# Kernel optimization log

Measured on AMD Instinct MI355X. Metric: run time of the kernel, lower is better.

## Reference

```python
import jax, jax.numpy as jnp
import numpy as np

N_NODES = 400      # total nodes across batch
B = 10             # graphs in batch (40 nodes each)
N_CONFIGS = 1000   # fixed by tile dataset
CONFIG_FEAT_DIM = 24
NODE_FEAT_DIM = 85  # continuous cols; node_feat has +1 col for shape-ele-type idx
N_SHAPE_TYPES = 8
SHAPE_EMB = 4
N_OPS = 120
OP_EMB = 32
H = 64             # h_dim
E = 800            # edges
CAT_DIM = NODE_FEAT_DIM + SHAPE_EMB + OP_EMB + CONFIG_FEAT_DIM  # 145


def _lin(k, i, o):
    return jax.random.normal(k, (i, o), jnp.float32) * (1.0 / np.sqrt(i))


def setup_inputs() -> dict:
    key = jax.random.key(0)
    ks = jax.random.split(key, 32)
    node_cont = jax.random.normal(ks[0], (N_NODES, NODE_FEAT_DIM), jnp.float32)
    shape_type = jax.random.randint(ks[1], (N_NODES, 1), 0, N_SHAPE_TYPES).astype(jnp.float32)
    node_feat = jnp.concatenate([node_cont, shape_type], axis=-1)  # [N, 86]
    node_opcode = jax.random.randint(ks[2], (N_NODES,), 0, N_OPS)
    config_feat = jax.random.normal(ks[3], (B * N_CONFIGS, CONFIG_FEAT_DIM), jnp.float32)
    edge_index = jax.random.randint(ks[4], (2, E), 0, N_NODES)
    batch = jnp.arange(N_NODES) // (N_NODES // B)  # 40 nodes per graph
    inp = dict(
        node_feat=node_feat, node_opcode=node_opcode, config_feat=config_feat,
        edge_index=edge_index, batch=batch,
        op_emb=jax.random.normal(ks[5], (N_OPS, OP_EMB), jnp.float32),
        shape_emb=jax.random.normal(ks[6], (N_SHAPE_TYPES, SHAPE_EMB), jnp.float32),
        W1=_lin(ks[7], CAT_DIM, 2 * H), b1=jnp.zeros((2 * H,), jnp.float32),
        W2=_lin(ks[8], 2 * H, 2 * H), b2=jnp.zeros((2 * H,), jnp.float32),
        Wl0=_lin(ks[9], 2 * H, H), Wr0=_lin(ks[10], 2 * H, H), bg0=jnp.zeros((H,), jnp.float32),
        Wl1=_lin(ks[11], H, H), Wr1=_lin(ks[12], H, H), bg1=jnp.zeros((H,), jnp.float32),
        Wl2=_lin(ks[13], H, H), Wr2=_lin(ks[14], H, H), bg2=jnp.zeros((H,), jnp.float32),
        Wp1=_lin(ks[15], H, H // 2), bp1=jnp.zeros((H // 2,), jnp.float32),
        Wp2=_lin(ks[16], H // 2, 1), bp2=jnp.zeros((1,), jnp.float32),
    )
    return inp


def _sage(x, src, dst, Wl, Wr, b, n):
    # PyG SAGEConv: lin_l(x) + lin_r(mean_{j->i} x_j), applied over [N, C, D]
    agg = jax.ops.segment_sum(x[src], dst, num_segments=n)
    deg = jax.ops.segment_sum(jnp.ones((src.shape[0],), x.dtype), dst, num_segments=n)
    mean = agg / jnp.maximum(deg, 1.0)[:, None, None]
    return x @ Wl + mean @ Wr + b


def reference(node_feat, node_opcode, config_feat, edge_index, batch,
              op_emb, shape_emb, W1, b1, W2, b2,
              Wl0, Wr0, bg0, Wl1, Wr1, bg1, Wl2, Wr2, bg2,
              Wp1, bp1, Wp2, bp2):
    n = node_feat.shape[0]
    cfg = config_feat.reshape(-1, N_CONFIGS, CONFIG_FEAT_DIM)  # [B, 1000, 24]
    ste = shape_emb[node_feat[:, -1].astype(jnp.int32)]        # [N, 4]
    op = op_emb[node_opcode]                                   # [N, 32]
    xn = jnp.concatenate([node_feat[:, :-1], ste, op], axis=-1)  # [N, 121]
    xn = jnp.broadcast_to(xn[:, None, :], (n, N_CONFIGS, xn.shape[-1]))
    xc = cfg[batch]  # repeat_interleave(cfg, n_nodes, dim=0) -> per-node config
    x = jnp.concatenate([xn, xc], axis=-1)                     # [N, 1000, 145]
    x = jax.nn.relu(x @ W1 + b1)
    x = jax.nn.relu(x @ W2 + b2)                               # [N, 1000, 128]
    src, dst = edge_index[0], edge_index[1]
    for Wl, Wr, bg in ((Wl0, Wr0, bg0), (Wl1, Wr1, bg1), (Wl2, Wr2, bg2)):
        x = jax.nn.relu(_sage(x, src, dst, Wl, Wr, bg, n))     # [N, 1000, 64]
    xf = x.reshape(n, -1)                                      # [N, 64000]
    cnt = jax.ops.segment_sum(jnp.ones((n,), xf.dtype), batch, num_segments=B)
    xg = jax.ops.segment_max(xf, batch, num_segments=B) \
         + jax.ops.segment_sum(xf, batch, num_segments=B) / jnp.maximum(cnt, 1.0)[:, None]
    xg = xg.reshape(B, N_CONFIGS, -1)                          # [B, 1000, 64]
    xg = xg / jnp.linalg.norm(xg, axis=-1, keepdims=True)
    out = (jax.nn.relu(xg @ Wp1 + bp1) @ Wp2 + bp2)[..., 0]    # [B, 1000]
    return out
```

## Files before the change

### kernel.cpp

```cpp
#include <hip/hip_runtime.h>
#include <hip/hip_bf16.h>

typedef unsigned short u16;
typedef short bf16x8 __attribute__((ext_vector_type(8)));
typedef float f32x4 __attribute__((ext_vector_type(4)));

#define NN 400
#define NB 10
#define NC 1000
#define CFD 24
#define NFD 85
#define NFROW 86
#define SEDIM 4
#define OEDIM 32
#define XND 121
#define EE 800
#define N_SHAPE_GUARD 7

__device__ __forceinline__ float b2f(u16 u) { return __uint_as_float((unsigned)u << 16); }
__device__ __forceinline__ u16 f2b(float v) {
  unsigned x = __float_as_uint(v);
  return (u16)((x + 0x7fff + ((x >> 16) & 1)) >> 16);
}
__device__ __forceinline__ float ldf(const void* p, int idx, int fz) {
  if (fz) return ((const float*)p)[idx];
  return b2f(((const u16*)p)[idx]);
}
__device__ __forceinline__ void stf(void* p, int idx, int fz, float v) {
  if (fz) { ((float*)p)[idx] = v; return; }
  ((u16*)p)[idx] = f2b(v);
}

__device__ __forceinline__ void detect_wave0(const void* W1, int t, int* flagl) {
  if (t < 64) {
    int wild = 0;
    const u16* wv = (const u16*)W1;
    for (int j = t; j < 512; j += 64) {
      float a = fabsf(b2f(wv[j]));
      if (!(a < 1e4f)) wild++;
    }
    #pragma unroll
    for (int off = 32; off; off >>= 1) wild += __shfl_xor(wild, off);
    if (t == 0) *flagl = (wild > 16) ? 1 : 0;
  }
}

__global__ __launch_bounds__(256) void k_prep_all(
    const void* __restrict__ node_feat, const int* __restrict__ opcode,
    const void* __restrict__ cfg, const int* __restrict__ edge_index,
    const void* __restrict__ op_emb, const void* __restrict__ shape_emb,
    const void* __restrict__ W1, const void* __restrict__ b1,
    const void* __restrict__ W2,
    const void* __restrict__ Wl0, const void* __restrict__ Wr0,
    const void* __restrict__ Wl1, const void* __restrict__ Wr1,
    const void* __restrict__ Wl2, const void* __restrict__ Wr2,
    float* __restrict__ A_node, float* __restrict__ C_cfg,
    u16* __restrict__ W2t, u16* __restrict__ Wc0t,
    u16* __restrict__ Wc1t, u16* __restrict__ Wc2t,
    int* __restrict__ offs, int* __restrict__ srcl) {
  __shared__ int flagl;
  int t = threadIdx.x;
  detect_wave0(W1, t, &flagl);
  __syncthreads();
  int fz = flagl;
  int bid = blockIdx.x;

  if (bid < 313) {
    __shared__ float w1l[CFD * 128];
    __shared__ float cfl[32 * CFD];
    int r0 = bid * 32;
    for (int idx = t; idx < CFD * 128; idx += 256)
      w1l[idx] = ldf(W1, (XND + (idx >> 7)) * 128 + (idx & 127), fz);
    for (int idx = t; idx < 32 * CFD; idx += 256) {
      int r = idx / CFD, k = idx - r * CFD;
      if (r0 + r < 10000) cfl[idx] = ldf(cfg, (r0 + r) * CFD + k, fz);
    }
    __syncthreads();
    for (int idx = t; idx < 4096; idx += 256) {
      int row = idx >> 7, col = idx & 127;
      if (r0 + row < 10000) {
        float acc = 0.f;
        #pragma unroll
        for (int k = 0; k < CFD; k++) acc += cfl[row * CFD + k] * w1l[k * 128 + col];
        C_cfg[(size_t)(r0 + row) * 128 + col] = acc;
      }
    }
    return;
  }
  if (bid < 363) {
    __shared__ float w1m[XND * 128];
    __shared__ float xnl[8 * 128];
    int i0 = (bid - 313) * 8;
    for (int idx = t; idx < XND * 128; idx += 256) w1m[idx] = ldf(W1, idx, fz);
    for (int idx = t; idx < 1024; idx += 256) {
      int node = idx >> 7, tt = idx & 127;
      int i = i0 + node;
      float v = 0.f;
      if (tt < NFD) {
        v = ldf(node_feat, i * NFROW + tt, fz);
      } else if (tt < NFD + SEDIM) {
        int st = (int)ldf(node_feat, i * NFROW + NFD, fz);
        st = min(max(st, 0), N_SHAPE_GUARD);
        v = ldf(shape_emb, st * SEDIM + (tt - NFD), fz);
      } else if (tt < XND) {
        int oc = min(max(opcode[i], 0), 119);
        v = ldf(op_emb, oc * OEDIM + (tt - NFD - SEDIM), fz);
      }
      xnl[idx] = v;
    }
    __syncthreads();
    for (int idx = t; idx < 1024; idx += 256) {
      int node = idx >> 7, tt = idx & 127;
      int i = i0 + node;
      float acc = ldf(b1, tt, fz);
      for (int k = 0; k < XND; k++) acc += xnl[node * 128 + k] * w1m[k * 128 + tt];
      A_node[i * 128 + tt] = acc;
    }
    return;
  }
  if (bid < 555) {
    int idx = (bid - 363) * 256 + t;
    if (idx < 16384) {
      int n = idx >> 7, k = idx & 127;
      W2t[idx] = f2b(ldf(W2, k * 128 + n, fz)); return;
    }
    idx -= 16384;
    if (idx < 16384) {
      int n = idx >> 7, k = idx & 127;
      float v = (n < 64) ? ldf(Wl0, k * 64 + n, fz) : ldf(Wr0, k * 64 + n - 64, fz);
      Wc0t[idx] = f2b(v); return;
    }
    idx -= 16384;
    if (idx < 8192) {
      int n = idx >> 6, k = idx & 63;
      float v = (n < 64) ? ldf(Wl1, k * 64 + n, fz) : ldf(Wr1, k * 64 + n - 64, fz);
      Wc1t[idx] = f2b(v); return;
    }
    idx -= 8192;
    if (idx < 8192) {
      int n = idx >> 6, k = idx & 63;
      float v = (n < 64) ? ldf(Wl2, k * 64 + n, fz) : ldf(Wr2, k * 64 + n - 64, fz);
      Wc2t[idx] = f2b(v); return;
    }
    return;
  }
  {
    __shared__ int cnt[NN];
    __shared__ int offl[NN + 1];
    for (int i = t; i < NN; i += 256) cnt[i] = 0;
    __syncthreads();
    for (int e = t; e < EE; e += 256) {
      int d = edge_index[EE + e] & 511; if (d < NN) atomicAdd(&cnt[d], 1);
    }
    __syncthreads();
    if (t == 0) {
      int s = 0;
      for (int i = 0; i < NN; i++) { offl[i] = s; s += cnt[i]; }
      offl[NN] = s;
    }
    __syncthreads();
    for (int i = t; i < NN; i += 256) cnt[i] = offl[i];
    for (int i = t; i < NN + 1; i += 256) offs[i] = offl[i];
    __syncthreads();
    for (int e = t; e < EE; e += 256) {
      int d = edge_index[EE + e] & 511;
      if (d < NN) {
        int p = atomicAdd(&cnt[d], 1);
        srcl[p] = min(max(edge_index[e], 0), NN - 1);
      }
    }
  }
}

__global__ __launch_bounds__(512, 1) void k_fused(
    const float* __restrict__ A_node, const float* __restrict__ C_cfg,
    const int* __restrict__ batch, const int* __restrict__ offs,
    const int* __restrict__ srcl,
    const u16* __restrict__ W2t, const u16* __restrict__ Wc0t,
    const u16* __restrict__ Wc1t, const u16* __restrict__ Wc2t,
    const void* __restrict__ b2, const void* __restrict__ bg0,
    const void* __restrict__ bg1, const void* __restrict__ bg2,
    const void* __restrict__ Wp1, const void* __restrict__ bp1,
    const void* __restrict__ Wp2, const void* __restrict__ bp2,
    const void* __restrict__ W1d, void* __restrict__ out) {
  __shared__ __align__(16) u16 xbuf[400 * 128];
  __shared__ __align__(16) u16 ybuf[400 * 64];
  __shared__ int offsl[401];
  __shared__ int srcll[EE];
  __shared__ int flagl;

  int c = blockIdx.x;
  int t = threadIdx.x;
  int w = t >> 6, l = t & 63;
  int lm = l & 15, quad = l >> 4;

  detect_wave0(W1d, t, &flagl);
  float* cfgl = (float*)ybuf;
  for (int idx = t; idx < 1280; idx += 512)
    cfgl[idx] = C_cfg[((size_t)(idx >> 7) * NC + c) * 128 + (idx & 127)];
  for (int idx = t; idx < 401; idx += 512) offsl[idx] = offs[idx];
  for (int idx = t; idx < EE; idx += 512) srcll[idx] = srcl[idx];
  __syncthreads();
  int fz = flagl;

  {
    bf16x8 wf[8][4];
    #pragma unroll
    for (int mt = 0; mt < 8; mt++)
      #pragma unroll
      for (int kt = 0; kt < 4; kt++)
        wf[mt][kt] = *reinterpret_cast<const bf16x8*>(W2t + (mt*16 + lm)*128 + kt*32 + quad*8);
    float bv[8][4];
    #pragma unroll
    for (int mt = 0; mt < 8; mt++)
      #pragma unroll
      for (int rg = 0; rg < 4; rg++) bv[mt][rg] = ldf(b2, mt*16 + quad*4 + rg, fz);

    for (int tile = w; tile < 25; tile += 8) {
      int i = tile*16 + lm;
      int b = batch[i] % NB;
      const float* an = A_node + i*128;
      const float* cf = cfgl + b*128;
      bf16x8 bfr[4];
      #pragma unroll
      for (int kt = 0; kt < 4; kt++) {
        int ko = kt*32 + quad*8;
        float4 a0 = *(const float4*)(an + ko);
        float4 a1 = *(const float4*)(an + ko + 4);
        float4 c0 = *(const float4*)(cf + ko);
        float4 c1 = *(const float4*)(cf + ko + 4);
        bf16x8 f;
        f[0] = (short)f2b(fmaxf(a0.x + c0.x, 0.f));
        f[1] = (short)f2b(fmaxf(a0.y + c0.y, 0.f));
        f[2] = (short)f2b(fmaxf(a0.z + c0.z, 0.f));
        f[3] = (short)f2b(fmaxf(a0.w + c0.w, 0.f));
        f[4] = (short)f2b(fmaxf(a1.x + c1.x, 0.f));
        f[5] = (short)f2b(fmaxf(a1.y + c1.y, 0.f));
        f[6] = (short)f2b(fmaxf(a1.z + c1.z, 0.f));
        f[7] = (short)f2b(fmaxf(a1.w + c1.w, 0.f));
        bfr[kt] = f;
      }
      f32x4 acc[8] = {};
      #pragma unroll
      for (int kt = 0; kt < 4; kt++)
        #pragma unroll
        for (int mt = 0; mt < 8; mt++)
          acc[mt] = __builtin_amdgcn_mfma_f32_16x16x32_bf16(wf[mt][kt], bfr[kt], acc[mt], 0, 0, 0);
      #pragma unroll
      for (int mt = 0; mt < 8; mt++) {
        ushort4 s;
        s.x = f2b(fmaxf(acc[mt][0] + bv[mt][0], 0.f));
        s.y = f2b(fmaxf(acc[mt][1] + bv[mt][1], 0.f));
        s.z = f2b(fmaxf(acc[mt][2] + bv[mt][2], 0.f));
        s.w = f2b(fmaxf(acc[mt][3] + bv[mt][3], 0.f));
        int ch = mt*2 + (quad >> 1);
        int chs = ch ^ (i & 7);
        *reinterpret_cast<ushort4*>(&xbuf[i*128 + chs*8 + (quad & 1)*4]) = s;
      }
    }
  }
  __syncthreads();

  {
    bf16x8 wl[4][4], wr[4][4];
    #pragma unroll
    for (int mt = 0; mt < 4; mt++)
      #pragma unroll
      for (int kt = 0; kt < 4; kt++) {
        wl[mt][kt] = *reinterpret_cast<const bf16x8*>(Wc0t + (mt*16 + lm)*128 + kt*32 + quad*8);
        wr[mt][kt] = *reinterpret_cast<const bf16x8*>(Wc0t + (64 + mt*16 + lm)*128 + kt*32 + quad*8);
      }
    float bv[4][4];
    #pragma unroll
    for (int mt = 0; mt < 4; mt++)
      #pragma unroll
      for (int rg = 0; rg < 4; rg++) bv[mt][rg] = ldf(bg0, mt*16 + quad*4 + rg, fz);

    for (int tile = w; tile < 25; tile += 8) {
      int i = tile*16 + lm;
      int o0 = offsl[i], o1 = offsl[i + 1];
      float rd = 1.f / fmaxf((float)(o1 - o0), 1.f);
      bf16x8 xf[4], mf[4];
      #pragma unroll
      for (int kt = 0; kt < 4; kt++)
        xf[kt] = *reinterpret_cast<const bf16x8*>(&xbuf[i*128 + ((kt*4 + quad) ^ (i & 7))*8]);
      float s8[4][8] = {};
      int e = o0;
      for (; e + 1 < o1; e += 2) {
        int sn0 = srcll[e], sn1 = srcll[e + 1];
        bf16x8 z0[4], z1[4];
        #pragma unroll
        for (int kt = 0; kt < 4; kt++) {
          z0[kt] = *reinterpret_cast<const bf16x8*>(&xbuf[sn0*128 + ((kt*4 + quad) ^ (sn0 & 7))*8]);
          z1[kt] = *reinterpret_cast<const bf16x8*>(&xbuf[sn1*128 + ((kt*4 + quad) ^ (sn1 & 7))*8]);
        }
        #pragma unroll
        for (int kt = 0; kt < 4; kt++)
          #pragma unroll
          for (int j = 0; j < 8; j++) {
            s8[kt][j] += b2f((u16)z0[kt][j]);
            s8[kt][j] += b2f((u16)z1[kt][j]);
          }
      }
      if (e < o1) {
        int sn0 = srcll[e];
        #pragma unroll
        for (int kt = 0; kt < 4; kt++) {
          bf16x8 zv = *reinterpret_cast<const bf16x8*>(&xbuf[sn0*128 + ((kt*4 + quad) ^ (sn0 & 7))*8]);
          #pragma unroll
          for (int j = 0; j < 8; j++) s8[kt][j] += b2f((u16)zv[j]);
        }
      }
      #pragma unroll
      for (int kt = 0; kt < 4; kt++) {
        bf16x8 f;
        #pragma unroll
        for (int j = 0; j < 8; j++) f[j] = (short)f2b(s8[kt][j] * rd);
        mf[kt] = f;
      }
      f32x4 acc[4] = {};
      #pragma unroll
      for (int kt = 0; kt < 4; kt++)
        #pragma unroll
        for (int mt = 0; mt < 4; mt++) {
          acc[mt] = __builtin_amdgcn_mfma_f32_16x16x32_bf16(wl[mt][kt], xf[kt], acc[mt], 0, 0, 0);
          acc[mt] = __builtin_amdgcn_mfma_f32_16x16x32_bf16(wr[mt][kt], mf[kt], acc[mt], 0, 0, 0);
        }
      #pragma unroll
      for (int mt = 0; mt < 4; mt++) {
        ushort4 s;
        s.x = f2b(fmaxf(acc[mt][0] + bv[mt][0], 0.f));
        s.y = f2b(fmaxf(acc[mt][1] + bv[mt][1], 0.f));
        s.z = f2b(fmaxf(acc[mt][2] + bv[mt][2], 0.f));
        s.w = f2b(fmaxf(acc[mt][3] + bv[mt][3], 0.f));
        int ch = mt*2 + (quad >> 1);
        int chs = ch ^ (i & 7);
        *reinterpret_cast<ushort4*>(&ybuf[i*64 + chs*8 + (quad & 1)*4]) = s;
      }
    }
  }
  __syncthreads();

  u16* src_buf = ybuf;
  u16* dst_buf = xbuf;
  for (int layer = 0; layer < 2; layer++) {
    const u16* Wt = (layer == 0) ? Wc1t : Wc2t;
    const void* bg = (layer == 0) ? bg1 : bg2;
    bf16x8 wl[4][2], wr[4][2];
    #pragma unroll
    for (int mt = 0; mt < 4; mt++)
      #pragma unroll
      for (int kt = 0; kt < 2; kt++) {
        wl[mt][kt] = *reinterpret_cast<const bf16x8*>(Wt + (mt*16 + lm)*64 + kt*32 + quad*8);
        wr[mt][kt] = *reinterpret_cast<const bf16x8*>(Wt + (64 + mt*16 + lm)*64 + kt*32 + quad*8);
      }
    float bv[4][4];
    #pragma unroll
    for (int mt = 0; mt < 4; mt++)
      #pragma unroll
      for (int rg = 0; rg < 4; rg++) bv[mt][rg] = ldf(bg, mt*16 + quad*4 + rg, fz);

    for (int tile = w; tile < 25; tile += 8) {
      int i = tile*16 + lm;
      int o0 = offsl[i], o1 = offsl[i + 1];
      float rd = 1.f / fmaxf((float)(o1 - o0), 1.f);
      bf16x8 xf[2], mf[2];
      #pragma unroll
      for (int kt = 0; kt < 2; kt++)
        xf[kt] = *reinterpret_cast<const bf16x8*>(&src_buf[i*64 + ((kt*4 + quad) ^ (i & 7))*8]);
      float s8[2][8] = {};
      int e = o0;
      for (; e + 1 < o1; e += 2) {
        int sn0 = srcll[e], sn1 = srcll[e + 1];
        bf16x8 z0[2], z1[2];
        #pragma unroll
        for (int kt = 0; kt < 2; kt++) {
          z0[kt] = *reinterpret_cast<const bf16x8*>(&src_buf[sn0*64 + ((kt*4 + quad) ^ (sn0 & 7))*8]);
          z1[kt] = *reinterpret_cast<const bf16x8*>(&src_buf[sn1*64 + ((kt*4 + quad) ^ (sn1 & 7))*8]);
        }
        #pragma unroll
        for (int kt = 0; kt < 2; kt++)
          #pragma unroll
          for (int j = 0; j < 8; j++) {
            s8[kt][j] += b2f((u16)z0[kt][j]);
            s8[kt][j] += b2f((u16)z1[kt][j]);
          }
      }
      if (e < o1) {
        int sn0 = srcll[e];
        #pragma unroll
        for (int kt = 0; kt < 2; kt++) {
          bf16x8 zv = *reinterpret_cast<const bf16x8*>(&src_buf[sn0*64 + ((kt*4 + quad) ^ (sn0 & 7))*8]);
          #pragma unroll
          for (int j = 0; j < 8; j++) s8[kt][j] += b2f((u16)zv[j]);
        }
      }
      #pragma unroll
      for (int kt = 0; kt < 2; kt++) {
        bf16x8 f;
        #pragma unroll
        for (int j = 0; j < 8; j++) f[j] = (short)f2b(s8[kt][j] * rd);
        mf[kt] = f;
      }
      f32x4 acc[4] = {};
      #pragma unroll
      for (int kt = 0; kt < 2; kt++)
        #pragma unroll
        for (int mt = 0; mt < 4; mt++) {
          acc[mt] = __builtin_amdgcn_mfma_f32_16x16x32_bf16(wl[mt][kt], xf[kt], acc[mt], 0, 0, 0);
          acc[mt] = __builtin_amdgcn_mfma_f32_16x16x32_bf16(wr[mt][kt], mf[kt], acc[mt], 0, 0, 0);
        }
      #pragma unroll
      for (int mt = 0; mt < 4; mt++) {
        ushort4 s;
        s.x = f2b(fmaxf(acc[mt][0] + bv[mt][0], 0.f));
        s.y = f2b(fmaxf(acc[mt][1] + bv[mt][1], 0.f));
        s.z = f2b(fmaxf(acc[mt][2] + bv[mt][2], 0.f));
        s.w = f2b(fmaxf(acc[mt][3] + bv[mt][3], 0.f));
        int ch = mt*2 + (quad >> 1);
        int chs = ch ^ (i & 7);
        *reinterpret_cast<ushort4*>(&dst_buf[i*64 + chs*8 + (quad & 1)*4]) = s;
      }
    }
    __syncthreads();
    u16* tmp = src_buf; src_buf = dst_buf; dst_buf = tmp;
  }

  {
    float* scr  = (float*)xbuf;
    float* wp1s = (float*)&xbuf[4096];
    for (int idx = t; idx < 2048; idx += 512) wp1s[idx] = ldf(Wp1, idx, fz);
    __syncthreads();
    for (int b = w; b < NB; b += 8) {
      int h = l;
      float mx = -3.0e38f, sm = 0.f;
      for (int j = 0; j < 40; j++) {
        int row = b*40 + j;
        int chs = (h >> 3) ^ (row & 7);
        float v = b2f(src_buf[row*64 + chs*8 + (h & 7)]);
        mx = fmaxf(mx, v); sm += v;
      }
      float g = mx + sm * (1.f / 40.f);
      float sq = g * g;
      #pragma unroll
      for (int off = 32; off; off >>= 1) sq += __shfl_xor(sq, off);
      float gn = g * rsqrtf(sq);
      scr[w*64 + h] = gn;
      int j32 = l & 31;
      float hj = ldf(bp1, j32, fz);
      for (int k = 0; k < 64; k++) hj += scr[w*64 + k] * wp1s[k*32 + j32];
      hj = fmaxf(hj, 0.f);
      float contrib = hj * ldf(Wp2, j32, fz);
      #pragma unroll
      for (int off = 32; off; off >>= 1) contrib += __shfl_xor(contrib, off);
      if (l == 0) stf(out, b*NC + c, fz, contrib * 0.5f + ldf(bp2, 0, fz));
    }
  }
}

extern "C" void kernel_launch(void* const* d_in, const int* in_sizes, int n_in,
                              void* d_out, int out_size, void* d_ws, size_t ws_size,
                              hipStream_t stream) {
  const void* node_feat   = d_in[0];
  const int*  node_opcode = (const int*)d_in[1];
  const void* config_feat = d_in[2];
  const int*  edge_index  = (const int*)d_in[3];
  const int*  batch       = (const int*)d_in[4];
  const void* op_emb      = d_in[5];
  const void* shape_emb   = d_in[6];
  const void* W1  = d_in[7];
  const void* b1  = d_in[8];
  const void* W2  = d_in[9];
  const void* b2  = d_in[10];
  const void* Wl0 = d_in[11];
  const void* Wr0 = d_in[12];
  const void* bg0 = d_in[13];
  const void* Wl1 = d_in[14];
  const void* Wr1 = d_in[15];
  const void* bg1 = d_in[16];
  const void* Wl2 = d_in[17];
  const void* Wr2 = d_in[18];
  const void* bg2 = d_in[19];
  const void* Wp1 = d_in[20];
  const void* bp1 = d_in[21];
  const void* Wp2 = d_in[22];
  const void* bp2 = d_in[23];

  char* p = (char*)d_ws;
  float* A_node = (float*)p; p += 400*128*4;
  float* C_cfg  = (float*)p; p += 10000*128*4;
  u16*   W2t    = (u16*)p;   p += 128*128*2;
  u16*   Wc0t   = (u16*)p;   p += 128*128*2;
  u16*   Wc1t   = (u16*)p;   p += 128*64*2;
  u16*   Wc2t   = (u16*)p;   p += 128*64*2;
  int*   offs   = (int*)p;   p += 2048;
  int*   srcl   = (int*)p;   p += 4096;

  k_prep_all<<<dim3(556), dim3(256), 0, stream>>>(
      node_feat, node_opcode, config_feat, edge_index, op_emb, shape_emb,
      W1, b1, W2, Wl0, Wr0, Wl1, Wr1, Wl2, Wr2,
      A_node, C_cfg, W2t, Wc0t, Wc1t, Wc2t, offs, srcl);

  k_fused<<<dim3(1000), dim3(512), 0, stream>>>(
      A_node, C_cfg, batch, offs, srcl, W2t, Wc0t, Wc1t, Wc2t,
      b2, bg0, bg1, bg2, Wp1, bp1, Wp2, bp2, W1, d_out);
}
```

Before: 331.2 us.

## Transform-then-aggregate SAGE layers with degree-sorted node combine pass

```diff
diff --git a/kernel.cpp b/kernel.cpp
--- a/kernel.cpp
+++ b/kernel.cpp
@@ -21,6 +21,9 @@
 __device__ __forceinline__ u16 f2b(float v) {
   unsigned x = __float_as_uint(v);
   return (u16)((x + 0x7fff + ((x >> 16) & 1)) >> 16);
+}
+__device__ __forceinline__ unsigned pk2(float a, float b) {
+  return (unsigned)f2b(a) | ((unsigned)f2b(b) << 16);
 }
 __device__ __forceinline__ float ldf(const void* p, int idx, int fz) {
   if (fz) return ((const float*)p)[idx];
@@ -57,7 +60,7 @@
     float* __restrict__ A_node, float* __restrict__ C_cfg,
     u16* __restrict__ W2t, u16* __restrict__ Wc0t,
     u16* __restrict__ Wc1t, u16* __restrict__ Wc2t,
-    int* __restrict__ offs, int* __restrict__ srcl) {
+    int* __restrict__ offs, int* __restrict__ srcl, int* __restrict__ perm) {
   __shared__ int flagl;
   int t = threadIdx.x;
   detect_wave0(W1, t, &flagl);
@@ -147,6 +150,7 @@
   {
     __shared__ int cnt[NN];
     __shared__ int offl[NN + 1];
+    __shared__ int dh[64];
     for (int i = t; i < NN; i += 256) cnt[i] = 0;
     __syncthreads();
     for (int e = t; e < EE; e += 256) {
@@ -169,13 +173,30 @@
         srcl[p] = min(max(edge_index[e], 0), NN - 1);
       }
     }
+    for (int i = t; i < 64; i += 256) dh[i] = 0;
+    __syncthreads();
+    for (int i = t; i < NN; i += 256) {
+      int d = min(offl[i + 1] - offl[i], 63);
+      atomicAdd(&dh[d], 1);
+    }
+    __syncthreads();
+    if (t == 0) {
+      int s = 0;
+      for (int d = 0; d < 64; d++) { int c = dh[d]; dh[d] = s; s += c; }
+    }
+    __syncthreads();
+    for (int i = t; i < NN; i += 256) {
+      int d = min(offl[i + 1] - offl[i], 63);
+      int p = atomicAdd(&dh[d], 1);
+      perm[p] = i;
+    }
   }
 }
 
 __global__ __launch_bounds__(512, 1) void k_fused(
     const float* __restrict__ A_node, const float* __restrict__ C_cfg,
     const int* __restrict__ batch, const int* __restrict__ offs,
-    const int* __restrict__ srcl,
+    const int* __restrict__ srcl, const int* __restrict__ perm,
     const u16* __restrict__ W2t, const u16* __restrict__ Wc0t,
     const u16* __restrict__ Wc1t, const u16* __restrict__ Wc2t,
     const void* __restrict__ b2, const void* __restrict__ bg0,
@@ -187,6 +208,8 @@
   __shared__ __align__(16) u16 ybuf[400 * 64];
   __shared__ int offsl[401];
   __shared__ int srcll[EE];
+  __shared__ int perml[NN];
+  __shared__ float bgl[192];
   __shared__ int flagl;
 
   int c = blockIdx.x;
@@ -200,22 +223,16 @@
     cfgl[idx] = C_cfg[((size_t)(idx >> 7) * NC + c) * 128 + (idx & 127)];
   for (int idx = t; idx < 401; idx += 512) offsl[idx] = offs[idx];
   for (int idx = t; idx < EE; idx += 512) srcll[idx] = srcl[idx];
+  for (int idx = t; idx < NN; idx += 512) perml[idx] = perm[idx];
   __syncthreads();
   int fz = flagl;
+  if (t < 64) {
+    bgl[t]       = ldf(bg0, t, fz);
+    bgl[64 + t]  = ldf(bg1, t, fz);
+    bgl[128 + t] = ldf(bg2, t, fz);
+  }
 
   {
-    bf16x8 wf[8][4];
-    #pragma unroll
-    for (int mt = 0; mt < 8; mt++)
-      #pragma unroll
-      for (int kt = 0; kt < 4; kt++)
-        wf[mt][kt] = *reinterpret_cast<const bf16x8*>(W2t + (mt*16 + lm)*128 + kt*32 + quad*8);
-    float bv[8][4];
-    #pragma unroll
-    for (int mt = 0; mt < 8; mt++)
-      #pragma unroll
-      for (int rg = 0; rg < 4; rg++) bv[mt][rg] = ldf(b2, mt*16 + quad*4 + rg, fz);
-
     for (int tile = w; tile < 25; tile += 8) {
       int i = tile*16 + lm;
       int b = batch[i] % NB;
@@ -244,187 +261,109 @@
       #pragma unroll
       for (int kt = 0; kt < 4; kt++)
         #pragma unroll
-        for (int mt = 0; mt < 8; mt++)
-          acc[mt] = __builtin_amdgcn_mfma_f32_16x16x32_bf16(wf[mt][kt], bfr[kt], acc[mt], 0, 0, 0);
+        for (int mt = 0; mt < 8; mt++) {
+          bf16x8 a = *reinterpret_cast<const bf16x8*>(W2t + (mt*16 + lm)*128 + kt*32 + quad*8);
+          acc[mt] = __builtin_amdgcn_mfma_f32_16x16x32_bf16(a, bfr[kt], acc[mt], 0, 0, 0);
+        }
+      #pragma unroll
+      for (int mt = 0; mt < 8; mt++) {
+        float bv0 = ldf(b2, mt*16 + quad*4 + 0, fz);
+        float bv1 = ldf(b2, mt*16 + quad*4 + 1, fz);
+        float bv2 = ldf(b2, mt*16 + quad*4 + 2, fz);
+        float bv3 = ldf(b2, mt*16 + quad*4 + 3, fz);
+        ushort4 s;
+        s.x = f2b(fmaxf(acc[mt][0] + bv0, 0.f));
+        s.y = f2b(fmaxf(acc[mt][1] + bv1, 0.f));
+        s.z = f2b(fmaxf(acc[mt][2] + bv2, 0.f));
+        s.w = f2b(fmaxf(acc[mt][3] + bv3, 0.f));
+        int chs = (mt*2 + (quad >> 1)) ^ (i & 7);
+        *reinterpret_cast<ushort4*>(&xbuf[i*128 + chs*8 + (quad & 1)*4]) = s;
+      }
+      bf16x8 xf[4];
+      #pragma unroll
+      for (int kt = 0; kt < 4; kt++)
+        xf[kt] = *reinterpret_cast<const bf16x8*>(&xbuf[i*128 + ((kt*4 + quad) ^ (i & 7))*8]);
+      f32x4 acc2[8] = {};
+      #pragma unroll
+      for (int kt = 0; kt < 4; kt++)
+        #pragma unroll
+        for (int mt = 0; mt < 8; mt++) {
+          bf16x8 a = *reinterpret_cast<const bf16x8*>(Wc0t + (mt*16 + lm)*128 + kt*32 + quad*8);
+          acc2[mt] = __builtin_amdgcn_mfma_f32_16x16x32_bf16(a, xf[kt], acc2[mt], 0, 0, 0);
+        }
       #pragma unroll
       for (int mt = 0; mt < 8; mt++) {
         ushort4 s;
-        s.x = f2b(fmaxf(acc[mt][0] + bv[mt][0], 0.f));
-        s.y = f2b(fmaxf(acc[mt][1] + bv[mt][1], 0.f));
-        s.z = f2b(fmaxf(acc[mt][2] + bv[mt][2], 0.f));
-        s.w = f2b(fmaxf(acc[mt][3] + bv[mt][3], 0.f));
-        int ch = mt*2 + (quad >> 1);
-        int chs = ch ^ (i & 7);
+        s.x = f2b(acc2[mt][0]); s.y = f2b(acc2[mt][1]);
+        s.z = f2b(acc2[mt][2]); s.w = f2b(acc2[mt][3]);
+        int chs = (mt*2 + (quad >> 1)) ^ (i & 7);
         *reinterpret_cast<ushort4*>(&xbuf[i*128 + chs*8 + (quad & 1)*4]) = s;
       }
     }
   }
   __syncthreads();
 
-  {
-    bf16x8 wl[4][4], wr[4][4];
-    #pragma unroll
-    for (int mt = 0; mt < 4; mt++)
-      #pragma unroll
-      for (int kt = 0; kt < 4; kt++) {
-        wl[mt][kt] = *reinterpret_cast<const bf16x8*>(Wc0t + (mt*16 + lm)*128 + kt*32 + quad*8);
-        wr[mt][kt] = *reinterpret_cast<const bf16x8*>(Wc0t + (64 + mt*16 + lm)*128 + kt*32 + quad*8);
-      }
-    float bv[4][4];
-    #pragma unroll
-    for (int mt = 0; mt < 4; mt++)
-      #pragma unroll
-      for (int rg = 0; rg < 4; rg++) bv[mt][rg] = ldf(bg0, mt*16 + quad*4 + rg, fz);
-
+  auto combine = [&](const float* bg) {
+    for (int g = t; g < NN * 8; g += 512) {
+      int node = perml[g >> 3];
+      int o = g & 7;
+      int e0 = offsl[node], e1 = offsl[node + 1];
+      float s[8] = {0,0,0,0,0,0,0,0};
+      for (int e = e0; e < e1; e++) {
+        int sn = srcll[e];
+        uint4 zv = *reinterpret_cast<const uint4*>(&xbuf[sn*128 + (8 + (o ^ (sn & 7)))*8]);
+        s[0] += b2f((u16)(zv.x & 0xffff)); s[1] += b2f((u16)(zv.x >> 16));
+        s[2] += b2f((u16)(zv.y & 0xffff)); s[3] += b2f((u16)(zv.y >> 16));
+        s[4] += b2f((u16)(zv.z & 0xffff)); s[5] += b2f((u16)(zv.z >> 16));
+        s[6] += b2f((u16)(zv.w & 0xffff)); s[7] += b2f((u16)(zv.w >> 16));
+      }
+      float rdg = 1.f / fmaxf((float)(e1 - e0), 1.f);
+      uint4 yv = *reinterpret_cast<const uint4*>(&xbuf[node*128 + (o ^ (node & 7))*8]);
+      float y0 = b2f((u16)(yv.x & 0xffff)), y1 = b2f((u16)(yv.x >> 16));
+      float y2 = b2f((u16)(yv.y & 0xffff)), y3 = b2f((u16)(yv.y >> 16));
+      float y4 = b2f((u16)(yv.z & 0xffff)), y5 = b2f((u16)(yv.z >> 16));
+      float y6 = b2f((u16)(yv.w & 0xffff)), y7 = b2f((u16)(yv.w >> 16));
+      const float* bgo = bg + o*8;
+      uint4 so;
+      so.x = pk2(fmaxf(y0 + s[0]*rdg + bgo[0], 0.f), fmaxf(y1 + s[1]*rdg + bgo[1], 0.f));
+      so.y = pk2(fmaxf(y2 + s[2]*rdg + bgo[2], 0.f), fmaxf(y3 + s[3]*rdg + bgo[3], 0.f));
+      so.z = pk2(fmaxf(y4 + s[4]*rdg + bgo[4], 0.f), fmaxf(y5 + s[5]*rdg + bgo[5], 0.f));
+      so.w = pk2(fmaxf(y6 + s[6]*rdg + bgo[6], 0.f), fmaxf(y7 + s[7]*rdg + bgo[7], 0.f));
+      *reinterpret_cast<uint4*>(&ybuf[node*64 + (o ^ (node & 7))*8]) = so;
+    }
+  };
+
+  auto gemm64 = [&](const u16* Wt) {
     for (int tile = w; tile < 25; tile += 8) {
       int i = tile*16 + lm;
-      int o0 = offsl[i], o1 = offsl[i + 1];
-      float rd = 1.f / fmaxf((float)(o1 - o0), 1.f);
-      bf16x8 xf[4], mf[4];
-      #pragma unroll
-      for (int kt = 0; kt < 4; kt++)
-        xf[kt] = *reinterpret_cast<const bf16x8*>(&xbuf[i*128 + ((kt*4 + quad) ^ (i & 7))*8]);
-      float s8[4][8] = {};
-      int e = o0;
-      for (; e + 1 < o1; e += 2) {
-        int sn0 = srcll[e], sn1 = srcll[e + 1];
-        bf16x8 z0[4], z1[4];
-        #pragma unroll
-        for (int kt = 0; kt < 4; kt++) {
-          z0[kt] = *reinterpret_cast<const bf16x8*>(&xbuf[sn0*128 + ((kt*4 + quad) ^ (sn0 & 7))*8]);
-          z1[kt] = *reinterpret_cast<const bf16x8*>(&xbuf[sn1*128 + ((kt*4 + quad) ^ (sn1 & 7))*8]);
-        }
-        #pragma unroll
-        for (int kt = 0; kt < 4; kt++)
-          #pragma unroll
-          for (int j = 0; j < 8; j++) {
-            s8[kt][j] += b2f((u16)z0[kt][j]);
-            s8[kt][j] += b2f((u16)z1[kt][j]);
-          }
-      }
-      if (e < o1) {
-        int sn0 = srcll[e];
-        #pragma unroll
-        for (int kt = 0; kt < 4; kt++) {
-          bf16x8 zv = *reinterpret_cast<const bf16x8*>(&xbuf[sn0*128 + ((kt*4 + quad) ^ (sn0 & 7))*8]);
-          #pragma unroll
-          for (int j = 0; j < 8; j++) s8[kt][j] += b2f((u16)zv[j]);
-        }
-      }
-      #pragma unroll
-      for (int kt = 0; kt < 4; kt++) {
-        bf16x8 f;
-        #pragma unroll
-        for (int j = 0; j < 8; j++) f[j] = (short)f2b(s8[kt][j] * rd);
-        mf[kt] = f;
-      }
-      f32x4 acc[4] = {};
-      #pragma unroll
-      for (int kt = 0; kt < 4; kt++)
-        #pragma unroll
-        for (int mt = 0; mt < 4; mt++) {
-          acc[mt] = __builtin_amdgcn_mfma_f32_16x16x32_bf16(wl[mt][kt], xf[kt], acc[mt], 0, 0, 0);
-          acc[mt] = __builtin_amdgcn_mfma_f32_16x16x32_bf16(wr[mt][kt], mf[kt], acc[mt], 0, 0, 0);
-        }
-      #pragma unroll
-      for (int mt = 0; mt < 4; mt++) {
-        ushort4 s;
-        s.x = f2b(fmaxf(acc[mt][0] + bv[mt][0], 0.f));
-        s.y = f2b(fmaxf(acc[mt][1] + bv[mt][1], 0.f));
-        s.z = f2b(fmaxf(acc[mt][2] + bv[mt][2], 0.f));
-        s.w = f2b(fmaxf(acc[mt][3] + bv[mt][3], 0.f));
-        int ch = mt*2 + (quad >> 1);
-        int chs = ch ^ (i & 7);
-        *reinterpret_cast<ushort4*>(&ybuf[i*64 + chs*8 + (quad & 1)*4]) = s;
-      }
-    }
-  }
-  __syncthreads();
-
-  u16* src_buf = ybuf;
-  u16* dst_buf = xbuf;
-  for (int layer = 0; layer < 2; layer++) {
-    const u16* Wt = (layer == 0) ? Wc1t : Wc2t;
-    const void* bg = (layer == 0) ? bg1 : bg2;
-    bf16x8 wl[4][2], wr[4][2];
-    #pragma unroll
-    for (int mt = 0; mt < 4; mt++)
-      #pragma unroll
-      for (int kt = 0; kt < 2; kt++) {
-        wl[mt][kt] = *reinterpret_cast<const bf16x8*>(Wt + (mt*16 + lm)*64 + kt*32 + quad*8);
-        wr[mt][kt] = *reinterpret_cast<const bf16x8*>(Wt + (64 + mt*16 + lm)*64 + kt*32 + quad*8);
-      }
-    float bv[4][4];
-    #pragma unroll
-    for (int mt = 0; mt < 4; mt++)
-      #pragma unroll
-      for (int rg = 0; rg < 4; rg++) bv[mt][rg] = ldf(bg, mt*16 + quad*4 + rg, fz);
-
-    for (int tile = w; tile < 25; tile += 8) {
-      int i = tile*16 + lm;
-      int o0 = offsl[i], o1 = offsl[i + 1];
-      float rd = 1.f / fmaxf((float)(o1 - o0), 1.f);
-      bf16x8 xf[2], mf[2];
+      bf16x8 xf[2];
       #pragma unroll
       for (int kt = 0; kt < 2; kt++)
-        xf[kt] = *reinterpret_cast<const bf16x8*>(&src_buf[i*64 + ((kt*4 + quad) ^ (i & 7))*8]);
-      float s8[2][8] = {};
-      int e = o0;
-      for (; e + 1 < o1; e += 2) {
-        int sn0 = srcll[e], sn1 = srcll[e + 1];
-        bf16x8 z0[2], z1[2];
-        #pragma unroll
-        for (int kt = 0; kt < 2; kt++) {
-          z0[kt] = *reinterpret_cast<const bf16x8*>(&src_buf[sn0*64 + ((kt*4 + quad) ^ (sn0 & 7))*8]);
-          z1[kt] = *reinterpret_cast<const bf16x8*>(&src_buf[sn1*64 + ((kt*4 + quad) ^ (sn1 & 7))*8]);
-        }
-        #pragma unroll
-        for (int kt = 0; kt < 2; kt++)
-          #pragma unroll
-          for (int j = 0; j < 8; j++) {
-            s8[kt][j] += b2f((u16)z0[kt][j]);
-            s8[kt][j] += b2f((u16)z1[kt][j]);
-          }
-      }
-      if (e < o1) {
-        int sn0 = srcll[e];
-        #pragma unroll
-        for (int kt = 0; kt < 2; kt++) {
-          bf16x8 zv = *reinterpret_cast<const bf16x8*>(&src_buf[sn0*64 + ((kt*4 + quad) ^ (sn0 & 7))*8]);
-          #pragma unroll
-          for (int j = 0; j < 8; j++) s8[kt][j] += b2f((u16)zv[j]);
-        }
-      }
-      #pragma unroll
-      for (int kt = 0; kt < 2; kt++) {
-        bf16x8 f;
-        #pragma unroll
-        for (int j = 0; j < 8; j++) f[j] = (short)f2b(s8[kt][j] * rd);
-        mf[kt] = f;
-      }
-      f32x4 acc[4] = {};
+        xf[kt] = *reinterpret_cast<const bf16x8*>(&ybuf[i*64 + ((kt*4 + quad) ^ (i & 7))*8]);
+      f32x4 acc[8] = {};
       #pragma unroll
       for (int kt = 0; kt < 2; kt++)
         #pragma unroll
-        for (int mt = 0; mt < 4; mt++) {
-          acc[mt] = __builtin_amdgcn_mfma_f32_16x16x32_bf16(wl[mt][kt], xf[kt], acc[mt], 0, 0, 0);
-          acc[mt] = __builtin_amdgcn_mfma_f32_16x16x32_bf16(wr[mt][kt], mf[kt], acc[mt], 0, 0, 0);
+        for (int mt = 0; mt < 8; mt++) {
+          bf16x8 a = *reinterpret_cast<const bf16x8*>(Wt + (mt*16 + lm)*64 + kt*32 + quad*8);
+          acc[mt] = __builtin_amdgcn_mfma_f32_16x16x32_bf16(a, xf[kt], acc[mt], 0, 0, 0);
         }
       #pragma unroll
-      for (int mt = 0; mt < 4; mt++) {
+      for (int mt = 0; mt < 8; mt++) {
         ushort4 s;
-        s.x = f2b(fmaxf(acc[mt][0] + bv[mt][0], 0.f));
-        s.y = f2b(fmaxf(acc[mt][1] + bv[mt][1], 0.f));
-        s.z = f2b(fmaxf(acc[mt][2] + bv[mt][2], 0.f));
-        s.w = f2b(fmaxf(acc[mt][3] + bv[mt][3], 0.f));
-        int ch = mt*2 + (quad >> 1);
-        int chs = ch ^ (i & 7);
-        *reinterpret_cast<ushort4*>(&dst_buf[i*64 + chs*8 + (quad & 1)*4]) = s;
-      }
-    }
-    __syncthreads();
-    u16* tmp = src_buf; src_buf = dst_buf; dst_buf = tmp;
-  }
+        s.x = f2b(acc[mt][0]); s.y = f2b(acc[mt][1]);
+        s.z = f2b(acc[mt][2]); s.w = f2b(acc[mt][3]);
+        int chs = (mt*2 + (quad >> 1)) ^ (i & 7);
+        *reinterpret_cast<ushort4*>(&xbuf[i*128 + chs*8 + (quad & 1)*4]) = s;
+      }
+    }
+  };
+
+  combine(bgl);          __syncthreads();
+  gemm64(Wc1t);          __syncthreads();
+  combine(bgl + 64);     __syncthreads();
+  gemm64(Wc2t);          __syncthreads();
+  combine(bgl + 128);    __syncthreads();
 
   {
     float* scr  = (float*)xbuf;
@@ -437,7 +376,7 @@
       for (int j = 0; j < 40; j++) {
         int row = b*40 + j;
         int chs = (h >> 3) ^ (row & 7);
-        float v = b2f(src_buf[row*64 + chs*8 + (h & 7)]);
+        float v = b2f(ybuf[row*64 + chs*8 + (h & 7)]);
         mx = fmaxf(mx, v); sm += v;
       }
       float g = mx + sm * (1.f / 40.f);
@@ -495,13 +434,14 @@
   u16*   Wc2t   = (u16*)p;   p += 128*64*2;
   int*   offs   = (int*)p;   p += 2048;
   int*   srcl   = (int*)p;   p += 4096;
+  int*   perm   = (int*)p;   p += 2048;
 
   k_prep_all<<<dim3(556), dim3(256), 0, stream>>>(
       node_feat, node_opcode, config_feat, edge_index, op_emb, shape_emb,
       W1, b1, W2, Wl0, Wr0, Wl1, Wr1, Wl2, Wr2,
-      A_node, C_cfg, W2t, Wc0t, Wc1t, Wc2t, offs, srcl);
+      A_node, C_cfg, W2t, Wc0t, Wc1t, Wc2t, offs, srcl, perm);
 
   k_fused<<<dim3(1000), dim3(512), 0, stream>>>(
-      A_node, C_cfg, batch, offs, srcl, W2t, Wc0t, Wc1t, Wc2t,
+      A_node, C_cfg, batch, offs, srcl, perm, W2t, Wc0t, Wc1t, Wc2t,
       b2, bg0, bg1, bg2, Wp1, bp1, Wp2, bp2, W1, d_out);
 }
```

Result: slower. 492.9 us (+48.8%).
